# Performance work log

Hardware: AMD Instinct MI355X
Metric: run time of the kernel (lower is better)

The kernel has to match this reference:

```python
import jax, jax.numpy as jnp
import numpy as np

N, L, S = 512, 1024, 32   # batch, latent dim, spatial (S*S == L)
F = 32 * S * S            # flattened encoder conv features (last conv = 32 ch)
H = 512                   # hidden width of latent MLP heads


def _lrelu(x):
    return jnp.where(x >= 0, x, 0.01 * x)


def _bn(x):
    # BatchNorm2d in training mode, gamma=1, beta=0 (default init)
    m = x.mean((0, 2, 3), keepdims=True)
    v = x.var((0, 2, 3), keepdims=True)
    return (x - m) * jax.lax.rsqrt(v + 1e-5)


def _conv(x, w, b):
    y = jax.lax.conv_general_dilated(x, w, (1, 1), 'SAME',
                                     dimension_numbers=('NCHW', 'OIHW', 'NCHW'))
    return y + b[None, :, None, None]


def _block(x, w, b):
    return _lrelu(_bn(_conv(x, w, b)))


def setup_inputs() -> dict:
    key = jax.random.key(0)
    ks = jax.random.split(key, 16)
    r = lambda k, s, sc: jax.random.normal(k, s, jnp.float32) * sc
    return {
        'x': r(ks[0], (N, 1, S, S), 1.0),
        'eps_c': r(ks[1], (N, L), 1.0),
        'eps_s': r(ks[2], (N, L), 1.0),
        'enc_cw1': r(ks[3], (2, 32, 1, 3, 3), 0.1),   'enc_cb1': jnp.zeros((2, 32)),
        'enc_cw2': r(ks[4], (2, 64, 32, 3, 3), 0.05), 'enc_cb2': jnp.zeros((2, 64)),
        'enc_cw3': r(ks[5], (2, 32, 64, 3, 3), 0.05), 'enc_cb3': jnp.zeros((2, 32)),
        'enc_muW1': r(ks[6], (2, H, F), 0.005), 'enc_muB1': jnp.zeros((2, H)),
        'enc_muW2': r(ks[7], (2, L, H), 0.02),  'enc_muB2': jnp.zeros((2, L)),
        'enc_vaW1': r(ks[8], (2, H, F), 0.005), 'enc_vaB1': jnp.zeros((2, H)),
        'enc_vaW2': r(ks[9], (2, L, H), 0.02),  'enc_vaB2': jnp.zeros((2, L)),
        'dec_cw1': r(ks[10], (2, 32, 1, 3, 3), 0.1),   'dec_cb1': jnp.zeros((2, 32)),
        'dec_cw2': r(ks[11], (2, 64, 32, 3, 3), 0.05), 'dec_cb2': jnp.zeros((2, 64)),
        'dec_cw3': r(ks[12], (2, 1, 64, 3, 3), 0.05),  'dec_cb3': jnp.zeros((2, 1)),
    }


def reference(x, eps_c, eps_s,
              enc_cw1, enc_cb1, enc_cw2, enc_cb2, enc_cw3, enc_cb3,
              enc_muW1, enc_muB1, enc_muW2, enc_muB2,
              enc_vaW1, enc_vaB1, enc_vaW2, enc_vaB2,
              dec_cw1, dec_cb1, dec_cw2, dec_cb2, dec_cw3, dec_cb3):
    def encode(i):
        h = _block(x, enc_cw1[i], enc_cb1[i])
        h = _block(h, enc_cw2[i], enc_cb2[i])
        h = _block(h, enc_cw3[i], enc_cb3[i])
        f = h.reshape(N, -1)                                   # [N, F]
        mu = _lrelu(_lrelu(f @ enc_muW1[i].T + enc_muB1[i]) @ enc_muW2[i].T + enc_muB2[i])
        lv = _lrelu(_lrelu(f @ enc_vaW1[i].T + enc_vaB1[i]) @ enc_vaW2[i].T + enc_vaB2[i])
        return mu, lv                                          # each [N, L]

    def decode(z, i):
        h = z.reshape(N, 1, S, S)
        h = _block(h, dec_cw1[i], dec_cb1[i])
        h = _block(h, dec_cw2[i], dec_cb2[i])
        h = _block(h, dec_cw3[i], dec_cb3[i])
        return h.reshape(N, 1, S, S)

    class_mu, class_logvar = encode(0)
    style_mu, style_logvar = encode(1)

    # precision-weighted product-of-experts group evidence (vectorized)
    precision = jnp.exp(-style_logvar)                  # 1/var, [N, L]
    group_var = 1.0 / precision.sum(0)                  # [L]
    group_mu = (style_mu * precision).sum(0) * group_var  # [L]
    group_logvar = jnp.log(group_var)

    # reparameterize
    z_c = eps_c * jnp.exp(0.5 * class_logvar) + class_mu          # [N, L]
    z_s = eps_s * jnp.exp(0.5 * group_logvar)[None] + group_mu[None]  # [N, L]

    output_c = decode(z_c, 0)
    output_s = jax.nn.relu(decode(z_s, 1))
    output = output_c * output_s                        # [N, 1, S, S]

    kl1 = -0.5 * jnp.sum(1.0 + class_logvar) + 0.5 * (
        jnp.sum(class_mu ** 2) + jnp.sum(jnp.exp(class_logvar) ** 2))
    kl2 = -0.5 * jnp.sum(1.0 + group_logvar) + 0.5 * (
        jnp.sum(group_mu ** 2) + jnp.sum(jnp.exp(group_logvar) ** 2))
    recon = (jnp.exp(x) - jnp.exp(output)) ** 2
    loss = -kl1 + kl2 + recon                           # [N, 1, S, S]
    return loss, output
```

## Files before the change

kernel.cpp:

```cpp
#include <hip/hip_runtime.h>

constexpr int N_   = 512;
constexpr int PIX  = 1024;
constexpr int L_   = 1024;
constexpr int F_   = 32768;
constexpr int H_   = 512;
constexpr float IC_ = 1.0f / (float)(512 * 1024);

__device__ __forceinline__ float lrelu(float t) { return t >= 0.f ? t : 0.01f * t; }

using frag  = __attribute__((ext_vector_type(8))) short;
using f32x4 = __attribute__((ext_vector_type(4))) float;
using s4    = __attribute__((ext_vector_type(4))) short;

#define BAR() do {                                              \
    asm volatile("s_waitcnt lgkmcnt(0)" ::: "memory");          \
    __builtin_amdgcn_s_barrier();                               \
    asm volatile("" ::: "memory");                              \
} while (0)

__device__ __forceinline__ void split_bf16(float v, short& hi, short& lo) {
    const unsigned b = __float_as_uint(v);
    hi = (short)(b >> 16);
    const float hf = __uint_as_float(b & 0xFFFF0000u);
    lo = (short)(__float_as_uint(v - hf) >> 16);
}

__device__ __forceinline__ frag ld2(const short* p) {
    union { frag f; struct { unsigned long long a, b; } u; } x;
    x.u.a = *(const unsigned long long*)(p);
    x.u.b = *(const unsigned long long*)(p + 4);
    return x.f;
}

__global__ __launch_bounds__(256) void wsplit6_kernel(
    const float* __restrict__ w0, const float* __restrict__ w1,
    const float* __restrict__ w2, const float* __restrict__ w3,
    const float* __restrict__ w4, const float* __restrict__ w5,
    short* __restrict__ hi, short* __restrict__ lo)
{
    const int layer = blockIdx.y;
    const float* W = layer == 0 ? w0 : layer == 1 ? w1 : layer == 2 ? w2 :
                     layer == 3 ? w3 : layer == 4 ? w4 : w5;
    const int CIN  = (layer == 1 || layer == 3) ? 64 : 32;
    const int NCOT = (layer == 1 || layer == 3) ? 2 : 4;
    const int idx = blockIdx.x * 256 + threadIdx.x;
    const int j    = idx & 7;
    const int lane = (idx >> 3) & 63;
    const int q    = lane >> 4, lm = lane & 15;
    const int blk  = idx >> 9;
    const int cot  = blk % NCOT;
    const int rest = blk / NCOT;
    const int pos  = rest % 9;
    const int cc   = rest / 9;
    const int co = cot * 16 + lm;
    const int ci = cc * 32 + q * 8 + j;
    short h, l;
    split_bf16(W[((size_t)co * CIN + ci) * 9 + pos], h, l);
    hi[layer * 18432 + idx] = h;
    lo[layer * 18432 + idx] = l;
}

template<int CIN, int COUT, bool BN_IN>
__global__ __launch_bounds__(256) void conv_mfma(
    const float* __restrict__ in, const short* __restrict__ wh,
    const short* __restrict__ wl, const float* __restrict__ bias,
    float* __restrict__ out, const float* __restrict__ stats_in,
    float* __restrict__ stats_out)
{
    constexpr int NCOT = COUT / 16;
    constexpr int NCH  = CIN / 32;
    constexpr int STR  = 36;
    constexpr int PLsh = 340 * STR;
    __shared__ __align__(16) short hiL[PLsh];
    __shared__ __align__(16) short loL[PLsh];
    __shared__ float red[2 * COUT];
    __shared__ float bnm[64], bni[64];
    const int tid  = threadIdx.x;
    const int n    = blockIdx.x >> 2;
    const int y0   = (blockIdx.x & 3) << 3;
    const int lane = tid & 63;
    const int wv   = tid >> 6;
    const int lm   = lane & 15;
    const int q    = lane >> 4;

    if (tid < 2 * COUT) red[tid] = 0.f;
    if (BN_IN && tid < CIN) {
        const float m  = stats_in[tid] * IC_;
        const float qq = stats_in[CIN + tid] * IC_;
        bnm[tid] = m;
        bni[tid] = rsqrtf(qq - m * m + 1e-5f);
    }
    __syncthreads();

    f32x4 acc[NCOT][4];
#pragma unroll
    for (int t = 0; t < NCOT; ++t)
#pragma unroll
        for (int pt = 0; pt < 4; ++pt) acc[t][pt] = {0.f, 0.f, 0.f, 0.f};

    const int rs0 = tid / 34, cs0 = tid % 34;
    const int idx1 = tid + 256;
    const int rs1 = idx1 / 34, cs1 = idx1 % 34;
    const int gr0 = y0 - 1 + rs0, gc0 = cs0 - 1;
    const int gr1 = y0 - 1 + rs1, gc1 = cs1 - 1;
    const bool in1 = idx1 < 340;
    const bool ok0 = ((unsigned)gr0 < 32u) && ((unsigned)gc0 < 32u);
    const bool ok1 = in1 && ((unsigned)gr1 < 32u) && ((unsigned)gc1 < 32u);
    const int  po0 = gr0 * 32 + gc0;
    const int  po1 = gr1 * 32 + gc1;

    const float* inb = in + ((size_t)n * CIN << 10);

    frag ahA[NCOT], alA[NCOT], ahB[NCOT], alB[NCOT];

    auto LDW = [&](frag (&dh)[NCOT], frag (&dl)[NCOT], int posAbs) {
#pragma unroll
        for (int t = 0; t < NCOT; ++t) {
            const size_t wb = (size_t)((posAbs * NCOT + t) * 512 + lane * 8);
            dh[t] = *(const frag*)&wh[wb];
            dl[t] = *(const frag*)&wl[wb];
        }
    };

    auto COMPUTE = [&](int pos, frag (&fh)[NCOT], frag (&fl)[NCOT]) {
        const int ky = pos / 3, kx = pos - ky * 3;
        __builtin_amdgcn_s_setprio(1);
#pragma unroll
        for (int pt = 0; pt < 4; ++pt) {
            const int ptile = wv * 4 + pt;
            const int row = ptile >> 1;
            const int col = ((ptile & 1) << 4) + lm;
            const int loff = ((row + ky) * 34 + col + kx) * STR + q * 8;
            const frag bh = ld2(&hiL[loff]);
            const frag bl = ld2(&loL[loff]);
#pragma unroll
            for (int t = 0; t < NCOT; ++t) {
                acc[t][pt] = __builtin_amdgcn_mfma_f32_16x16x32_bf16(
                    fh[t], bh, acc[t][pt], 0, 0, 0);
                acc[t][pt] = __builtin_amdgcn_mfma_f32_16x16x32_bf16(
                    fh[t], bl, acc[t][pt], 0, 0, 0);
                acc[t][pt] = __builtin_amdgcn_mfma_f32_16x16x32_bf16(
                    fl[t], bh, acc[t][pt], 0, 0, 0);
            }
        }
        __builtin_amdgcn_s_setprio(0);
    };

#pragma unroll 1
    for (int cc = 0; cc < NCH; ++cc) {
        if (cc) BAR();

        LDW(ahA, alA, cc * 9 + 0);

        {
            float v0r[32], v1r[32];
#pragma unroll
            for (int u = 0; u < 32; ++u) {
                const int cg = cc * 32 + u;
                v0r[u] = ok0 ? inb[((size_t)cg << 10) + po0] : 0.f;
                v1r[u] = ok1 ? inb[((size_t)cg << 10) + po1] : 0.f;
            }
#pragma unroll
            for (int u4 = 0; u4 < 32; u4 += 4) {
                s4 h0v, l0v, h1v, l1v;
#pragma unroll
                for (int e = 0; e < 4; ++e) {
                    const int ci = u4 + e;
                    const int cg = cc * 32 + ci;
                    float v0 = v0r[ci];
                    if (BN_IN && ok0) v0 = lrelu((v0 - bnm[cg]) * bni[cg]);
                    short h, l;
                    split_bf16(v0, h, l);
                    h0v[e] = h; l0v[e] = l;
                    float v1 = v1r[ci];
                    if (BN_IN && ok1) v1 = lrelu((v1 - bnm[cg]) * bni[cg]);
                    short h1, l1;
                    split_bf16(v1, h1, l1);
                    h1v[e] = h1; l1v[e] = l1;
                }
                *(s4*)&hiL[tid * STR + u4] = h0v;
                *(s4*)&loL[tid * STR + u4] = l0v;
                if (in1) {
                    *(s4*)&hiL[idx1 * STR + u4] = h1v;
                    *(s4*)&loL[idx1 * STR + u4] = l1v;
                }
            }
        }
        BAR();

#pragma unroll 1
        for (int pos = 0; pos < 8; pos += 2) {
            LDW(ahB, alB, cc * 9 + pos + 1);
            COMPUTE(pos, ahA, alA);
            LDW(ahA, alA, cc * 9 + pos + 2);
            COMPUTE(pos + 1, ahB, alB);
        }
        COMPUTE(8, ahA, alA);
    }

    float* ob = out + ((size_t)n * COUT << 10);
#pragma unroll
    for (int t = 0; t < NCOT; ++t) {
#pragma unroll
        for (int r = 0; r < 4; ++r) {
            const int co = t * 16 + q * 4 + r;
            const float b = bias[co];
            float s = 0.f, sq = 0.f;
#pragma unroll
            for (int pt = 0; pt < 4; ++pt) {
                const float v = acc[t][pt][r] + b;
                ob[((size_t)co << 10) + (y0 << 5) + ((wv * 4 + pt) << 4) + lm] = v;
                s += v; sq += v * v;
            }
#pragma unroll
            for (int off = 8; off > 0; off >>= 1) {
                s  += __shfl_down(s, off, 64);
                sq += __shfl_down(sq, off, 64);
            }
            if (lm == 0) {
                atomicAdd(&red[co], s);
                atomicAdd(&red[COUT + co], sq);
            }
        }
    }
    __syncthreads();
    if (tid < 2 * COUT) atomicAdd(&stats_out[tid], red[tid]);
}

template<int CIN, int COPB, bool BN_IN>
__global__ __launch_bounds__(256) void conv3x3(
    const float* __restrict__ in, const float* __restrict__ w,
    const float* __restrict__ bias, float* __restrict__ out,
    const float* __restrict__ stats_in, float* __restrict__ stats_out,
    int Cout)
{
    constexpr int CT = (CIN < 4) ? CIN : 4;
    __shared__ float tile[CT * PIX];
    __shared__ float red[2 * COPB];
    const int groups = Cout / COPB;
    const int n   = blockIdx.x / groups;
    const int co0 = (blockIdx.x % groups) * COPB;
    const int tid = threadIdx.x;
    const int x   = tid & 31;
    const int y0  = (tid >> 5) * 4;

    float acc[COPB][4];
#pragma unroll
    for (int c = 0; c < COPB; ++c)
#pragma unroll
        for (int j = 0; j < 4; ++j) acc[c][j] = 0.f;

    const float* inbase = in + (size_t)n * CIN * PIX;

#pragma unroll 1
    for (int s0 = 0; s0 < CIN; s0 += CT) {
        __syncthreads();
#pragma unroll
        for (int s = 0; s < CT; ++s) {
            float4 v = ((const float4*)(inbase + (size_t)(s0 + s) * PIX))[tid];
            if (BN_IN) {
                const int c = s0 + s;
                const float m   = stats_in[c] * IC_;
                const float q   = stats_in[CIN + c] * IC_;
                const float inv = rsqrtf(q - m * m + 1e-5f);
                v.x = lrelu((v.x - m) * inv);
                v.y = lrelu((v.y - m) * inv);
                v.z = lrelu((v.z - m) * inv);
                v.w = lrelu((v.w - m) * inv);
            }
            ((float4*)tile)[s * 256 + tid] = v;
        }
        __syncthreads();
#pragma unroll 2
        for (int s = 0; s < CT; ++s) {
            const int ci = s0 + s;
            const float* tp = tile + s * PIX;
            float r[6][3];
#pragma unroll
            for (int ry = 0; ry < 6; ++ry) {
                const int yy = y0 + ry - 1;
                const bool yok = (unsigned)yy < 32u;
#pragma unroll
                for (int cx = 0; cx < 3; ++cx) {
                    const int xx = x + cx - 1;
                    const bool ok = yok && ((unsigned)xx < 32u);
                    r[ry][cx] = ok ? tp[yy * 32 + xx] : 0.f;
                }
            }
#pragma unroll
            for (int c = 0; c < COPB; ++c) {
                const float* wp = w + ((size_t)(co0 + c) * CIN + ci) * 9;
#pragma unroll
                for (int ky = 0; ky < 3; ++ky)
#pragma unroll
                    for (int kx = 0; kx < 3; ++kx) {
                        const float wv = wp[ky * 3 + kx];
#pragma unroll
                        for (int j = 0; j < 4; ++j)
                            acc[c][j] += r[ky + j][kx] * wv;
                    }
            }
        }
    }

    if (tid < 2 * COPB) red[tid] = 0.f;
    __syncthreads();
#pragma unroll
    for (int c = 0; c < COPB; ++c) {
        const float b = bias[co0 + c];
        float* ob = out + (((size_t)n * Cout + co0 + c) << 10);
        float s = 0.f, q = 0.f;
#pragma unroll
        for (int j = 0; j < 4; ++j) {
            const float v = acc[c][j] + b;
            ob[(y0 + j) * 32 + x] = v;
            s += v; q += v * v;
        }
#pragma unroll
        for (int off = 32; off > 0; off >>= 1) {
            s += __shfl_down(s, off, 64);
            q += __shfl_down(q, off, 64);
        }
        if ((tid & 63) == 0) {
            atomicAdd(&red[c], s);
            atomicAdd(&red[COPB + c], q);
        }
    }
    __syncthreads();
    if (tid < COPB)
        atomicAdd(&stats_out[co0 + tid], red[tid]);
    else if (tid < 2 * COPB)
        atomicAdd(&stats_out[Cout + co0 + tid - COPB], red[tid]);
}

template<int MODE>
__global__ __launch_bounds__(256) void gemm_mfma(
    const float* __restrict__ A0, const float* __restrict__ A1,
    const float* __restrict__ B0, const float* __restrict__ B1,
    float* __restrict__ C0, float* __restrict__ C1,
    int K, int Nh, int kchunk, int xph,
    const float* __restrict__ bnstats, int Cin,
    const float* __restrict__ ba0, const float* __restrict__ ba1)
{
    __shared__ short AhL[8192], AlL[8192], BhL[8192], BlL[8192];
    const int tid  = threadIdx.x;
    const int head = blockIdx.x / xph;
    const int n0   = (blockIdx.x % xph) * 128;
    const int m0   = blockIdx.y * 128;
    const float* A = head ? A1 : A0;
    const float* B = head ? B1 : B0;
    float*       C = head ? C1 : C0;
    const float* BA = head ? ba1 : ba0;
    const int k0 = blockIdx.z * kchunk;

    const int lane = tid & 63;
    const int wv   = tid >> 6;
    const int wm   = wv & 1;
    const int wn   = wv >> 1;
    const int lm   = lane & 15;
    const int q    = lane >> 4;

    const int srow = tid >> 1;
    const int smt  = srow >> 4;
    const int slm  = srow & 15;
    const int sq0  = (tid & 1) * 2;
    const int ks   = (tid & 1) * 16;

    float bnm0 = 0.f, bni0 = 1.f, bnm1 = 0.f, bni1 = 1.f;
    if (MODE == 1) {
        const int c0 = k0 >> 10;
        bnm0 = bnstats[c0] * IC_;
        const float q0 = bnstats[Cin + c0] * IC_;
        bni0 = rsqrtf(q0 - bnm0 * bnm0 + 1e-5f);
        const int c1 = (c0 + 1 < Cin) ? c0 + 1 : c0;
        bnm1 = bnstats[c1] * IC_;
        const float q1 = bnstats[Cin + c1] * IC_;
        bni1 = rsqrtf(q1 - bnm1 * bnm1 + 1e-5f);
    }

    f32x4 acc[4][4];
#pragma unroll
    for (int i = 0; i < 4; ++i)
#pragma unroll
        for (int j = 0; j < 4; ++j) acc[i][j] = {0.f, 0.f, 0.f, 0.f};

    auto cv8 = [](float4 u, float4 w2, frag& h, frag& l) {
        const float v[8] = {u.x, u.y, u.z, u.w, w2.x, w2.y, w2.z, w2.w};
#pragma unroll
        for (int e = 0; e < 8; ++e) {
            short hh, ll;
            split_bf16(v[e], hh, ll);
            h[e] = hh; l[e] = ll;
        }
    };

    float4 a4[4], b4[4];
    auto LOADAB = [&](int kb) {
        const float* Ap = A + (size_t)(m0 + srow) * K + kb + ks;
        const float* Bp = B + (size_t)(n0 + srow) * K + kb + ks;
#pragma unroll
        for (int g = 0; g < 4; ++g) a4[g] = ((const float4*)Ap)[g];
#pragma unroll
        for (int g = 0; g < 4; ++g) b4[g] = ((const float4*)Bp)[g];
    };

    const int o0 = ((smt * 4 + sq0) * 16 + slm) * 8;
    const int o1 = ((smt * 4 + sq0 + 1) * 16 + slm) * 8;

    auto STAGE = [&](int s) {
        if (MODE == 1) {
            const int sel = s >> 5;
            const float m   = sel ? bnm1 : bnm0;
            const float inv = sel ? bni1 : bni0;
#pragma unroll
            for (int g = 0; g < 4; ++g) {
                a4[g].x = lrelu((a4[g].x - m) * inv);
                a4[g].y = lrelu((a4[g].y - m) * inv);
                a4[g].z = lrelu((a4[g].z - m) * inv);
                a4[g].w = lrelu((a4[g].w - m) * inv);
            }
        }
        if (MODE == 2) {
            const float* bp = BA + k0 + s * 32 + ks;
#pragma unroll
            for (int g = 0; g < 4; ++g) {
                const float4 bv = ((const float4*)bp)[g];
                a4[g].x = lrelu(a4[g].x + bv.x);
                a4[g].y = lrelu(a4[g].y + bv.y);
                a4[g].z = lrelu(a4[g].z + bv.z);
                a4[g].w = lrelu(a4[g].w + bv.w);
            }
        }
        frag ah0, al0, ah1, al1, bh0, bl0, bh1, bl1;
        cv8(a4[0], a4[1], ah0, al0);
        cv8(a4[2], a4[3], ah1, al1);
        cv8(b4[0], b4[1], bh0, bl0);
        cv8(b4[2], b4[3], bh1, bl1);
        const int pb = (s & 1) << 12;
        *(frag*)&AhL[pb + o0] = ah0;  *(frag*)&AhL[pb + o1] = ah1;
        *(frag*)&AlL[pb + o0] = al0;  *(frag*)&AlL[pb + o1] = al1;
        *(frag*)&BhL[pb + o0] = bh0;  *(frag*)&BhL[pb + o1] = bh1;
        *(frag*)&BlL[pb + o0] = bl0;  *(frag*)&BlL[pb + o1] = bl1;
    };

    auto MMA = [&](int s) {
        const int pb = (s & 1) << 12;
        frag fah[4], fal[4], fbh[4], fbl[4];
#pragma unroll
        for (int t = 0; t < 4; ++t) {
            const int oa = pb + (((wm * 4 + t) * 4 + q) * 16 + lm) * 8;
            const int ob = pb + (((wn * 4 + t) * 4 + q) * 16 + lm) * 8;
            fah[t] = *(const frag*)&AhL[oa];
            fal[t] = *(const frag*)&AlL[oa];
            fbh[t] = *(const frag*)&BhL[ob];
            fbl[t] = *(const frag*)&BlL[ob];
        }
        __builtin_amdgcn_s_setprio(1);
#pragma unroll
        for (int i = 0; i < 4; ++i)
#pragma unroll
            for (int j = 0; j < 4; ++j) {
                acc[i][j] = __builtin_amdgcn_mfma_f32_16x16x32_bf16(
                    fah[i], fbh[j], acc[i][j], 0, 0, 0);
                acc[i][j] = __builtin_amdgcn_mfma_f32_16x16x32_bf16(
                    fah[i], fbl[j], acc[i][j], 0, 0, 0);
                acc[i][j] = __builtin_amdgcn_mfma_f32_16x16x32_bf16(
                    fal[i], fbh[j], acc[i][j], 0, 0, 0);
            }
        __builtin_amdgcn_s_setprio(0);
    };

    const int T = kchunk >> 5;

    LOADAB(k0);
    STAGE(0);
    LOADAB(k0 + 32);
    BAR();

#pragma unroll 1
    for (int s = 1; s < T; ++s) {
        MMA(s - 1);
        STAGE(s);
        if (s + 1 < T) LOADAB(k0 + (s + 1) * 32);
        BAR();
    }
    MMA(T - 1);

#pragma unroll
    for (int i = 0; i < 4; ++i) {
        const int m = m0 + wm * 64 + i * 16 + q * 4;
#pragma unroll
        for (int j = 0; j < 4; ++j) {
            const int n = n0 + wn * 64 + j * 16 + lm;
            float* cp = C + (size_t)m * Nh + n;
#pragma unroll
            for (int r = 0; r < 4; ++r)
                atomicAdd(cp + (size_t)r * Nh, acc[i][j][r]);
        }
    }
}

__device__ __forceinline__ void block_reduce_atomic(float t, float* target)
{
#pragma unroll
    for (int off = 32; off > 0; off >>= 1) t += __shfl_down(t, off, 64);
    __shared__ float lt[4];
    const int wave = threadIdx.x >> 6, lane = threadIdx.x & 63;
    if (lane == 0) lt[wave] = t;
    __syncthreads();
    if (threadIdx.x == 0) atomicAdd(target, lt[0] + lt[1] + lt[2] + lt[3]);
}

__global__ __launch_bounds__(256) void poe_kernel(
    const float* __restrict__ mu1, const float* __restrict__ lv1,
    const float* __restrict__ bmu, const float* __restrict__ blv,
    float* __restrict__ gmu, float* __restrict__ glv, float* __restrict__ kl)
{
    const int l = blockIdx.x * 256 + threadIdx.x;
    const float bm = bmu[l], bl = blv[l];
    float sp = 0.f, sm = 0.f;
    for (int n = 0; n < N_; ++n) {
        const float lv = lrelu(lv1[(size_t)n * L_ + l] + bl);
        const float p  = expf(-lv);
        sp += p;
        sm += lrelu(mu1[(size_t)n * L_ + l] + bm) * p;
    }
    const float gv = 1.f / sp;
    const float gm = sm * gv;
    const float gl = -logf(sp);
    gmu[l] = gm;
    glv[l] = gl;
    const float t = -0.5f * (1.f + gl) + 0.5f * (gm * gm + gv * gv);
    block_reduce_atomic(t, &kl[1]);
}

__global__ __launch_bounds__(256) void reparam_kernel(
    const float* __restrict__ mu0, const float* __restrict__ lv0,
    const float* __restrict__ bmu, const float* __restrict__ blv,
    const float* __restrict__ eps_c, const float* __restrict__ eps_s,
    const float* __restrict__ gmu, const float* __restrict__ glv,
    float* __restrict__ zc, float* __restrict__ zs, float* __restrict__ kl)
{
    const int idx = blockIdx.x * 256 + threadIdx.x;
    const int l = idx & (L_ - 1);
    const float m  = lrelu(mu0[idx] + bmu[l]);
    const float lv = lrelu(lv0[idx] + blv[l]);
    zc[idx] = eps_c[idx] * expf(0.5f * lv) + m;
    zs[idx] = eps_s[idx] * expf(0.5f * glv[l]) + gmu[l];
    const float e = expf(lv);
    const float t = -0.5f * (1.f + lv) + 0.5f * (m * m + e * e);
    block_reduce_atomic(t, &kl[0]);
}

__global__ __launch_bounds__(256) void final_kernel(
    const float* __restrict__ x, const float* __restrict__ oc,
    const float* __restrict__ os, const float* __restrict__ stC,
    const float* __restrict__ stS, const float* __restrict__ kl,
    float* __restrict__ out)
{
    const int idx = blockIdx.x * 256 + threadIdx.x;
    const float mc = stC[0] * IC_, qc = stC[1] * IC_;
    const float ivc = rsqrtf(qc - mc * mc + 1e-5f);
    const float ms = stS[0] * IC_, qs = stS[1] * IC_;
    const float ivs = rsqrtf(qs - ms * ms + 1e-5f);
    const float tc = lrelu((oc[idx] - mc) * ivc);
    const float ts = fmaxf((os[idx] - ms) * ivs, 0.f);
    const float o = tc * ts;
    const float d = expf(x[idx]) - expf(o);
    out[idx]            = -kl[0] + kl[1] + d * d;
    out[N_ * PIX + idx] = o;
}

extern "C" void kernel_launch(void* const* d_in, const int* in_sizes, int n_in,
                              void* d_out, int out_size, void* d_ws, size_t ws_size,
                              hipStream_t stream)
{
    const float* x        = (const float*)d_in[0];
    const float* eps_c    = (const float*)d_in[1];
    const float* eps_s    = (const float*)d_in[2];
    const float* enc_cw1  = (const float*)d_in[3];
    const float* enc_cb1  = (const float*)d_in[4];
    const float* enc_cw2  = (const float*)d_in[5];
    const float* enc_cb2  = (const float*)d_in[6];
    const float* enc_cw3  = (const float*)d_in[7];
    const float* enc_cb3  = (const float*)d_in[8];
    const float* enc_muW1 = (const float*)d_in[9];
    const float* enc_muB1 = (const float*)d_in[10];
    const float* enc_muW2 = (const float*)d_in[11];
    const float* enc_muB2 = (const float*)d_in[12];
    const float* enc_vaW1 = (const float*)d_in[13];
    const float* enc_vaB1 = (const float*)d_in[14];
    const float* enc_vaW2 = (const float*)d_in[15];
    const float* enc_vaB2 = (const float*)d_in[16];
    const float* dec_cw1  = (const float*)d_in[17];
    const float* dec_cb1  = (const float*)d_in[18];
    const float* dec_cw2  = (const float*)d_in[19];
    const float* dec_cb2  = (const float*)d_in[20];
    const float* dec_cw3  = (const float*)d_in[21];
    const float* dec_cb3  = (const float*)d_in[22];
    float* out = (float*)d_out;

    float* ws   = (float*)d_ws;
    float* bufA = ws;
    float* bufB = bufA + (size_t)N_ * 64 * PIX;
    float* h1   = bufB + (size_t)N_ * 32 * PIX;
    float* h2   = h1 + N_ * H_;
    float* mu0  = h2 + N_ * H_;
    float* lv0  = mu0 + N_ * L_;
    float* mu1  = lv0 + N_ * L_;
    float* lv1  = mu1 + N_ * L_;
    float* zc   = lv1 + N_ * L_;
    float* zs   = zc + N_ * L_;
    float* oc   = zs + N_ * L_;
    float* os   = oc + N_ * L_;
    float* gmu  = os + N_ * L_;
    float* glv  = gmu + L_;
    float* stats = glv + L_;
    float* kl   = stats + 12 * 128;
    short* wsh  = (short*)(kl + 4);
    short* wsl  = wsh + 6 * 18432;

    auto st  = [&](int s) { return stats + 128 * s; };
    auto whp = [&](int layer) { return wsh + layer * 18432; };
    auto wlp = [&](int layer) { return wsl + layer * 18432; };

    hipMemsetAsync(stats, 0, (12 * 128 + 4) * sizeof(float), stream);

    wsplit6_kernel<<<dim3(72, 6), 256, 0, stream>>>(
        enc_cw2, enc_cw3, enc_cw2 + 64 * 32 * 9, enc_cw3 + 32 * 64 * 9,
        dec_cw2, dec_cw2 + 64 * 32 * 9, wsh, wsl);

    for (int i = 0; i < 2; ++i) {
        const float* cw1 = enc_cw1 + (size_t)i * 32 * 9;
        const float* cb1 = enc_cb1 + (size_t)i * 32;
        const float* cb2 = enc_cb2 + (size_t)i * 64;
        const float* cb3 = enc_cb3 + (size_t)i * 32;

        conv3x3<1, 16, false><<<N_ * 2, 256, 0, stream>>>(
            x, cw1, cb1, bufB, nullptr, st(i * 3 + 0), 32);
        conv_mfma<32, 64, true><<<N_ * 4, 256, 0, stream>>>(
            bufB, whp(i * 2), wlp(i * 2), cb2, bufA, st(i * 3 + 0), st(i * 3 + 1));
        conv_mfma<64, 32, true><<<N_ * 4, 256, 0, stream>>>(
            bufA, whp(i * 2 + 1), wlp(i * 2 + 1), cb3, bufB, st(i * 3 + 1), st(i * 3 + 2));

        const float* W1m = enc_muW1 + (size_t)i * H_ * F_;
        const float* B1m = enc_muB1 + (size_t)i * H_;
        const float* W2m = enc_muW2 + (size_t)i * L_ * H_;
        const float* W1v = enc_vaW1 + (size_t)i * H_ * F_;
        const float* B1v = enc_vaB1 + (size_t)i * H_;
        const float* W2v = enc_vaW2 + (size_t)i * L_ * H_;
        float* mu_i = (i == 0) ? mu0 : mu1;
        float* lv_i = (i == 0) ? lv0 : lv1;

        hipMemsetAsync(h1, 0, (size_t)2 * N_ * H_ * sizeof(float), stream);
        gemm_mfma<1><<<dim3(8, 4, 16), 256, 0, stream>>>(
            bufB, bufB, W1m, W1v, h1, h2, F_, H_, 2048, 4,
            st(i * 3 + 2), 32, nullptr, nullptr);

        hipMemsetAsync(mu_i, 0, (size_t)2 * N_ * L_ * sizeof(float), stream);
        gemm_mfma<2><<<dim3(16, 4, 4), 256, 0, stream>>>(
            h1, h2, W2m, W2v, mu_i, lv_i, H_, L_, 128, 8,
            nullptr, 0, B1m, B1v);
    }

    poe_kernel<<<L_ / 256, 256, 0, stream>>>(
        mu1, lv1, enc_muB2 + L_, enc_vaB2 + L_, gmu, glv, kl);
    reparam_kernel<<<(N_ * L_) / 256, 256, 0, stream>>>(
        mu0, lv0, enc_muB2, enc_vaB2, eps_c, eps_s, gmu, glv, zc, zs, kl);

    for (int i = 0; i < 2; ++i) {
        const float* cw1 = dec_cw1 + (size_t)i * 32 * 9;
        const float* cb1 = dec_cb1 + (size_t)i * 32;
        const float* cb2 = dec_cb2 + (size_t)i * 64;
        const float* cw3 = dec_cw3 + (size_t)i * 64 * 9;
        const float* cb3 = dec_cb3 + (size_t)i * 1;
        const float* zi = (i == 0) ? zc : zs;
        float* oi = (i == 0) ? oc : os;

        conv3x3<1, 16, false><<<N_ * 2, 256, 0, stream>>>(
            zi, cw1, cb1, bufB, nullptr, st(6 + i * 3 + 0), 32);
        conv_mfma<32, 64, true><<<N_ * 4, 256, 0, stream>>>(
            bufB, whp(4 + i), wlp(4 + i), cb2, bufA, st(6 + i * 3 + 0), st(6 + i * 3 + 1));
        conv3x3<64, 1, true><<<N_, 256, 0, stream>>>(
            bufA, cw3, cb3, oi, st(6 + i * 3 + 1), st(6 + i * 3 + 2), 1);
    }

    final_kernel<<<(N_ * PIX) / 256, 256, 0, stream>>>(
        x, oc, os, st(8), st(11), kl, out);
}
```

Before: 1.458 ms.

## Split conv_mfma output channels across two wave groups with 512-thread blocks

Raises the MFMA conv blocks from 256 to 512 threads. Waves 0-3 and 4-7 now take different halves of the output-channel tiles, so each wave keeps half as many accumulators and weight fragments in registers. The shared-memory input tile is now staged one pixel per thread, in two 16-channel chunks. The aim is more waves per CU and lower register pressure, at the cost of each wave reloading the B fragments from LDS for its own half of the channels.

```diff
diff --git a/kernel.cpp b/kernel.cpp
--- a/kernel.cpp
+++ b/kernel.cpp
@@ -62,14 +62,15 @@
 }
 
 template<int CIN, int COUT, bool BN_IN>
-__global__ __launch_bounds__(256) void conv_mfma(
+__global__ __launch_bounds__(512) void conv_mfma(
     const float* __restrict__ in, const short* __restrict__ wh,
     const short* __restrict__ wl, const float* __restrict__ bias,
     float* __restrict__ out, const float* __restrict__ stats_in,
     float* __restrict__ stats_out)
 {
-    constexpr int NCOT = COUT / 16;
-    constexpr int NCH  = CIN / 32;
+    constexpr int NCOT  = COUT / 16;
+    constexpr int NCOT2 = NCOT / 2;
+    constexpr int NCH   = CIN / 32;
     constexpr int STR  = 36;
     constexpr int PLsh = 340 * STR;
     __shared__ __align__(16) short hiL[PLsh];
@@ -81,6 +82,8 @@
     const int y0   = (blockIdx.x & 3) << 3;
     const int lane = tid & 63;
     const int wv   = tid >> 6;
+    const int pgrp = wv & 3;
+    const int cotg = wv >> 2;
     const int lm   = lane & 15;
     const int q    = lane >> 4;
 
@@ -93,49 +96,45 @@
     }
     __syncthreads();
 
-    f32x4 acc[NCOT][4];
-#pragma unroll
-    for (int t = 0; t < NCOT; ++t)
+    f32x4 acc[NCOT2][4];
+#pragma unroll
+    for (int t = 0; t < NCOT2; ++t)
 #pragma unroll
         for (int pt = 0; pt < 4; ++pt) acc[t][pt] = {0.f, 0.f, 0.f, 0.f};
 
     const int rs0 = tid / 34, cs0 = tid % 34;
-    const int idx1 = tid + 256;
-    const int rs1 = idx1 / 34, cs1 = idx1 % 34;
     const int gr0 = y0 - 1 + rs0, gc0 = cs0 - 1;
-    const int gr1 = y0 - 1 + rs1, gc1 = cs1 - 1;
-    const bool in1 = idx1 < 340;
-    const bool ok0 = ((unsigned)gr0 < 32u) && ((unsigned)gc0 < 32u);
-    const bool ok1 = in1 && ((unsigned)gr1 < 32u) && ((unsigned)gc1 < 32u);
+    const bool act = tid < 340;
+    const bool ok0 = act && ((unsigned)gr0 < 32u) && ((unsigned)gc0 < 32u);
     const int  po0 = gr0 * 32 + gc0;
-    const int  po1 = gr1 * 32 + gc1;
 
     const float* inb = in + ((size_t)n * CIN << 10);
 
-    frag ahA[NCOT], alA[NCOT], ahB[NCOT], alB[NCOT];
-
-    auto LDW = [&](frag (&dh)[NCOT], frag (&dl)[NCOT], int posAbs) {
-#pragma unroll
-        for (int t = 0; t < NCOT; ++t) {
-            const size_t wb = (size_t)((posAbs * NCOT + t) * 512 + lane * 8);
+    frag ahA[NCOT2], alA[NCOT2], ahB[NCOT2], alB[NCOT2];
+
+    auto LDW = [&](frag (&dh)[NCOT2], frag (&dl)[NCOT2], int posAbs) {
+#pragma unroll
+        for (int t = 0; t < NCOT2; ++t) {
+            const int cot = cotg * NCOT2 + t;
+            const size_t wb = (size_t)((posAbs * NCOT + cot) * 512 + lane * 8);
             dh[t] = *(const frag*)&wh[wb];
             dl[t] = *(const frag*)&wl[wb];
         }
     };
 
-    auto COMPUTE = [&](int pos, frag (&fh)[NCOT], frag (&fl)[NCOT]) {
+    auto COMPUTE = [&](int pos, frag (&fh)[NCOT2], frag (&fl)[NCOT2]) {
         const int ky = pos / 3, kx = pos - ky * 3;
         __builtin_amdgcn_s_setprio(1);
 #pragma unroll
         for (int pt = 0; pt < 4; ++pt) {
-            const int ptile = wv * 4 + pt;
+            const int ptile = pgrp * 4 + pt;
             const int row = ptile >> 1;
             const int col = ((ptile & 1) << 4) + lm;
             const int loff = ((row + ky) * 34 + col + kx) * STR + q * 8;
             const frag bh = ld2(&hiL[loff]);
             const frag bl = ld2(&loL[loff]);
 #pragma unroll
-            for (int t = 0; t < NCOT; ++t) {
+            for (int t = 0; t < NCOT2; ++t) {
                 acc[t][pt] = __builtin_amdgcn_mfma_f32_16x16x32_bf16(
                     fh[t], bh, acc[t][pt], 0, 0, 0);
                 acc[t][pt] = __builtin_amdgcn_mfma_f32_16x16x32_bf16(
@@ -153,37 +152,30 @@
 
         LDW(ahA, alA, cc * 9 + 0);
 
-        {
-            float v0r[32], v1r[32];
-#pragma unroll
-            for (int u = 0; u < 32; ++u) {
-                const int cg = cc * 32 + u;
+#pragma unroll 1
+        for (int cb = 0; cb < 32; cb += 16) {
+            float v0r[16];
+#pragma unroll
+            for (int u = 0; u < 16; ++u) {
+                const int cg = cc * 32 + cb + u;
                 v0r[u] = ok0 ? inb[((size_t)cg << 10) + po0] : 0.f;
-                v1r[u] = ok1 ? inb[((size_t)cg << 10) + po1] : 0.f;
-            }
-#pragma unroll
-            for (int u4 = 0; u4 < 32; u4 += 4) {
-                s4 h0v, l0v, h1v, l1v;
-#pragma unroll
-                for (int e = 0; e < 4; ++e) {
-                    const int ci = u4 + e;
-                    const int cg = cc * 32 + ci;
-                    float v0 = v0r[ci];
-                    if (BN_IN && ok0) v0 = lrelu((v0 - bnm[cg]) * bni[cg]);
-                    short h, l;
-                    split_bf16(v0, h, l);
-                    h0v[e] = h; l0v[e] = l;
-                    float v1 = v1r[ci];
-                    if (BN_IN && ok1) v1 = lrelu((v1 - bnm[cg]) * bni[cg]);
-                    short h1, l1;
-                    split_bf16(v1, h1, l1);
-                    h1v[e] = h1; l1v[e] = l1;
-                }
-                *(s4*)&hiL[tid * STR + u4] = h0v;
-                *(s4*)&loL[tid * STR + u4] = l0v;
-                if (in1) {
-                    *(s4*)&hiL[idx1 * STR + u4] = h1v;
-                    *(s4*)&loL[idx1 * STR + u4] = l1v;
+            }
+            if (act) {
+#pragma unroll
+                for (int u4 = 0; u4 < 16; u4 += 4) {
+                    s4 h0v, l0v;
+#pragma unroll
+                    for (int e = 0; e < 4; ++e) {
+                        const int ci = cb + u4 + e;
+                        const int cg = cc * 32 + ci;
+                        float v0 = v0r[u4 + e];
+                        if (BN_IN && ok0) v0 = lrelu((v0 - bnm[cg]) * bni[cg]);
+                        short h, l;
+                        split_bf16(v0, h, l);
+                        h0v[e] = h; l0v[e] = l;
+                    }
+                    *(s4*)&hiL[tid * STR + cb + u4] = h0v;
+                    *(s4*)&loL[tid * STR + cb + u4] = l0v;
                 }
             }
         }
@@ -201,16 +193,17 @@
 
     float* ob = out + ((size_t)n * COUT << 10);
 #pragma unroll
-    for (int t = 0; t < NCOT; ++t) {
+    for (int t = 0; t < NCOT2; ++t) {
 #pragma unroll
         for (int r = 0; r < 4; ++r) {
-            const int co = t * 16 + q * 4 + r;
+            const int co = (cotg * NCOT2 + t) * 16 + q * 4 + r;
             const float b = bias[co];
             float s = 0.f, sq = 0.f;
 #pragma unroll
             for (int pt = 0; pt < 4; ++pt) {
+                const int ptile = pgrp * 4 + pt;
                 const float v = acc[t][pt][r] + b;
-                ob[((size_t)co << 10) + (y0 << 5) + ((wv * 4 + pt) << 4) + lm] = v;
+                ob[((size_t)co << 10) + (y0 << 5) + (ptile << 4) + lm] = v;
                 s += v; sq += v * v;
             }
 #pragma unroll
@@ -639,9 +632,9 @@
 
         conv3x3<1, 16, false><<<N_ * 2, 256, 0, stream>>>(
             x, cw1, cb1, bufB, nullptr, st(i * 3 + 0), 32);
-        conv_mfma<32, 64, true><<<N_ * 4, 256, 0, stream>>>(
+        conv_mfma<32, 64, true><<<N_ * 4, 512, 0, stream>>>(
             bufB, whp(i * 2), wlp(i * 2), cb2, bufA, st(i * 3 + 0), st(i * 3 + 1));
-        conv_mfma<64, 32, true><<<N_ * 4, 256, 0, stream>>>(
+        conv_mfma<64, 32, true><<<N_ * 4, 512, 0, stream>>>(
             bufA, whp(i * 2 + 1), wlp(i * 2 + 1), cb3, bufB, st(i * 3 + 1), st(i * 3 + 2));
 
         const float* W1m = enc_muW1 + (size_t)i * H_ * F_;
@@ -680,7 +673,7 @@
 
         conv3x3<1, 16, false><<<N_ * 2, 256, 0, stream>>>(
             zi, cw1, cb1, bufB, nullptr, st(6 + i * 3 + 0), 32);
-        conv_mfma<32, 64, true><<<N_ * 4, 256, 0, stream>>>(
+        conv_mfma<32, 64, true><<<N_ * 4, 512, 0, stream>>>(
             bufB, whp(4 + i), wlp(4 + i), cb2, bufA, st(6 + i * 3 + 0), st(6 + i * 3 + 1));
         conv3x3<64, 1, true><<<N_, 256, 0, stream>>>(
             bufA, cw3, cb3, oi, st(6 + i * 3 + 1), st(6 + i * 3 + 2), 1);
```

Result: faster. 1.365 ms (-6.4%).
